# Kernel optimization log

Hardware: AMD Instinct MI355X
Metric: run time of the kernel (lower is better)

The kernel has to match this reference:

```python
import jax, jax.numpy as jnp
import numpy as np

IN_FF = 7  # joints
MASK = np.ones(9, dtype=np.float32)  # [P(3), RPY sin/cos (6)]


def _mlp(x, params):
    # params: list of (W, b); sigmoid after every layer except the last (predict)
    h = x
    for W, b in params[:-1]:
        h = jax.nn.sigmoid(h @ W + b)
    W, b = params[-1]
    return h @ W + b


def _rpy_head(x, params):
    # FeedForwardNet_RPY forward: y -> [sin(y0), cos(y1)], angle = atan2(sin, cos)
    y = _mlp(x, params)
    s = jnp.sin(y[..., 0])
    c = jnp.cos(y[..., 1])
    ang = jnp.arctan2(s, c)
    return jnp.stack([s, c, ang], axis=-1)  # (..., 3)


def setup_inputs():
    key = jax.random.key(0)
    ks = jax.random.split(key, 26)
    m = 16384
    d = {"x": jax.random.normal(ks[0], (m, 2 * IN_FF), jnp.float32)}

    def lin(k, fi, fo, name, i):
        k1, k2 = jax.random.split(k)
        lim = 1.0 / np.sqrt(fi)  # torch Linear default init
        d[name + "_W" + str(i)] = jax.random.uniform(k1, (fi, fo), jnp.float32, -lim, lim)
        d[name + "_b" + str(i)] = jax.random.uniform(k2, (fo,), jnp.float32, -lim, lim)

    idx = 1
    for name, dims in [("pos", [7, 512, 512, 3]), ("roll", [7, 256, 256, 2]),
                       ("pitch", [7, 256, 256, 2]), ("yaw", [7, 256, 256, 2])]:
        for i in range(3):
            lin(ks[idx], dims[i], dims[i + 1], name, i)
            idx += 1
    return d


def _forward(x, pos_p, roll_p, pitch_p, yaw_p):
    mask = jnp.asarray(MASK)
    M_P, M_RPY = mask[:3], mask[3:]
    q, qdot = x[:, :IN_FF], x[:, IN_FF:]

    # position net: forward + per-sample Jacobian (exact, replaces the autograd loop)
    P = _mlp(q, pos_p)                                          # (m, 3)
    J_P = jax.vmap(jax.jacfwd(lambda z: _mlp(z, pos_p)))(q)     # (m, 3, 7)
    vel = jnp.einsum("moi,mi->mo", J_P, qdot)                   # bmm(J_P, jointVels)
    P = P * M_P
    vel = vel * M_P

    heads = []
    for p in (roll_p, pitch_p, yaw_p):
        f = lambda z, p=p: _rpy_head(z, p)
        y = f(q)                                # (m, 3): [sin, cos, angle]
        J = jax.vmap(jax.jacfwd(f))(q)          # (m, 3, 7)
        v = jnp.einsum("moi,mi->mo", J[:, :2, :], qdot)  # (m, 2)
        heads.append((y, J, v))
    (yR, JR, vR), (yPi, JPi, vPi), (yY, JY, vY) = heads

    # order: [roll_sin, pitch_sin, yaw_sin, roll_cos, pitch_cos, yaw_cos]
    RPY = jnp.stack([yR[:, 0], yPi[:, 0], yY[:, 0], yR[:, 1], yPi[:, 1], yY[:, 1]], axis=1) * M_RPY
    vel_RPY = jnp.stack([vR[:, 0], vPi[:, 0], vY[:, 0], vR[:, 1], vPi[:, 1], vY[:, 1]], axis=1) * M_RPY
    J_RPY = jnp.stack([JR[:, 0], JPi[:, 0], JY[:, 0], JR[:, 1], JPi[:, 1], JY[:, 1]], axis=1)  # (m,6,7)

    out = jnp.concatenate([P, RPY, vel, vel_RPY], axis=1)            # (m, 18)
    J_tot = jnp.concatenate([J_P, J_RPY], axis=1)                    # (m, 9, 7)
    out_angles = jnp.concatenate([P, yR[:, 2:3], yPi[:, 2:3], yY[:, 2:3]], axis=1)       # (m, 6)
    J_tot_angles = jnp.concatenate([J_P, JR[:, 2:3], JPi[:, 2:3], JY[:, 2:3]], axis=1)   # (m, 6, 7)
    return out, J_tot, out_angles, J_tot_angles


def reference(x, pos_W0, pos_b0, pos_W1, pos_b1, pos_W2, pos_b2,
              roll_W0, roll_b0, roll_W1, roll_b1, roll_W2, roll_b2,
              pitch_W0, pitch_b0, pitch_W1, pitch_b1, pitch_W2, pitch_b2,
              yaw_W0, yaw_b0, yaw_W1, yaw_b1, yaw_W2, yaw_b2):
    pos_p = [(pos_W0, pos_b0), (pos_W1, pos_b1), (pos_W2, pos_b2)]
    roll_p = [(roll_W0, roll_b0), (roll_W1, roll_b1), (roll_W2, roll_b2)]
    pitch_p = [(pitch_W0, pitch_b0), (pitch_W1, pitch_b1), (pitch_W2, pitch_b2)]
    yaw_p = [(yaw_W0, yaw_b0), (yaw_W1, yaw_b1), (yaw_W2, yaw_b2)]
    return _forward(x, pos_p, roll_p, pitch_p, yaw_p)
```

## Files before the change

kernel.cpp:

```cpp
#include <hip/hip_runtime.h>
#include <math.h>

typedef __attribute__((ext_vector_type(8))) short short8;
typedef __attribute__((ext_vector_type(4))) float floatx4;

__device__ __forceinline__ float sig(float z) { return 1.0f / (1.0f + __expf(-z)); }

__device__ __forceinline__ unsigned short f2bf(float f) {
    unsigned u = __float_as_uint(f);
    u = (u + 0x7FFFu + ((u >> 16) & 1u)) >> 16;
    return (unsigned short)u;
}

__global__ void convert_w1(const float* __restrict__ src, unsigned short* __restrict__ dst,
                           int H, int logH) {
    int idx = blockIdx.x * 256 + threadIdx.x;
    if (idx >= H * H) return;
    int n = idx & (H - 1), k = idx >> logH;
    int KT = H >> 5;
    int blk = (n >> 4) * KT + (k >> 5);
    int lane = ((k >> 3) & 3) * 16 + (n & 15);
    int j = k & 7;
    dst[(blk * 64 + lane) * 8 + j] = f2bf(src[idx]);
}

__global__ __launch_bounds__(256, 2)
void pos_mfma(const float* __restrict__ x,
              const float* __restrict__ W0, const float* __restrict__ b0,
              const float* __restrict__ b1,
              const float* __restrict__ W2, const float* __restrict__ b2,
              const unsigned short* __restrict__ wsW1,
              float* __restrict__ out, int ns)
{
    extern __shared__ unsigned short sA[];
    __shared__ float sB0[512];
    __shared__ float sB1[512];
    __shared__ float sW2[1536];
    __shared__ float sQ[8][8];
    __shared__ float sQd[8][8];
    __shared__ float sAcc[4][64][3];
    __shared__ float sSum[64][3];

    const int tid = threadIdx.x;
    const int m0  = blockIdx.x * 8;

    for (int i = tid; i < 512;  i += 256) { sB0[i] = b0[i]; sB1[i] = b1[i]; }
    for (int i = tid; i < 1536; i += 256) sW2[i] = W2[i];
    if (tid < 112) {
        int m = tid / 14, c = tid % 14;
        float v = x[(m0 + m) * 14 + c];
        if (c < 7) sQ[m][c] = v; else sQd[m][c - 7] = v;
    }
    __syncthreads();

    const float4* W04 = (const float4*)W0;
    #pragma unroll
    for (int t = 0; t < 2; ++t) {
        int item = tid + t * 256;
        int s = item >> 6, k8 = item & 63;
        float q[7], w0v[7][8];
        #pragma unroll
        for (int i = 0; i < 7; i++) {
            q[i] = sQ[s][i];
            float4 a = W04[i * 128 + k8 * 2], b4 = W04[i * 128 + k8 * 2 + 1];
            w0v[i][0]=a.x; w0v[i][1]=a.y; w0v[i][2]=a.z; w0v[i][3]=a.w;
            w0v[i][4]=b4.x; w0v[i][5]=b4.y; w0v[i][6]=b4.z; w0v[i][7]=b4.w;
        }
        float hv[8], dv[8];
        #pragma unroll
        for (int jj = 0; jj < 8; jj++) {
            float z = sB0[k8 * 8 + jj];
            #pragma unroll
            for (int i = 0; i < 7; i++) z = fmaf(q[i], w0v[i][jj], z);
            float h = sig(z);
            hv[jj] = h; dv[jj] = h - h * h;
        }
        int kt = k8 >> 2, kq = k8 & 3, sw = kt & 7;
        int rr0 = s * 8;
        {
            short8 v;
            #pragma unroll
            for (int jj = 0; jj < 8; jj++) v[jj] = (short)f2bf(hv[jj]);
            *(short8*)&sA[((rr0 >> 4) * 16 + kt) * 512 + ((kq * 16 + (rr0 & 15)) ^ sw) * 8] = v;
        }
        #pragma unroll
        for (int i = 0; i < 7; i++) {
            int rr = rr0 + 1 + i;
            short8 v;
            #pragma unroll
            for (int jj = 0; jj < 8; jj++) v[jj] = (short)f2bf(dv[jj] * w0v[i][jj]);
            *(short8*)&sA[((rr >> 4) * 16 + kt) * 512 + ((kq * 16 + (rr & 15)) ^ sw) * 8] = v;
        }
    }
    __syncthreads();

    const int w = tid >> 6, lane = tid & 63;
    const int quad = lane >> 4, col = lane & 15;
    const int srcl = lane & 47;
    const floatx4 z4 = {0.f, 0.f, 0.f, 0.f};

    floatx4 acc[4][8];
    #pragma unroll
    for (int rt = 0; rt < 4; rt++)
        #pragma unroll
        for (int ct = 0; ct < 8; ct++) acc[rt][ct] = z4;

    const short8* bbase = (const short8*)wsW1 + (size_t)(w * 8 * 16) * 64 + lane;

    short8 bufA[8], bufB[8];
    #pragma unroll
    for (int ct = 0; ct < 8; ++ct) bufA[ct] = bbase[(ct * 16) * 64];

    for (int kt2 = 0; kt2 < 16; kt2 += 2) {
        #pragma unroll
        for (int ct = 0; ct < 8; ++ct) bufB[ct] = bbase[(ct * 16 + kt2 + 1) * 64];
        {
            const int kt = kt2, sw = kt & 7;
            short8 afr[4];
            #pragma unroll
            for (int rt = 0; rt < 4; ++rt)
                afr[rt] = *(const short8*)&sA[(rt * 16 + kt) * 512 + (lane ^ sw) * 8];
            #pragma unroll
            for (int ct = 0; ct < 8; ++ct)
                #pragma unroll
                for (int rt = 0; rt < 4; ++rt)
                    acc[rt][ct] = __builtin_amdgcn_mfma_f32_16x16x32_bf16(afr[rt], bufA[ct], acc[rt][ct], 0, 0, 0);
        }
        if (kt2 + 2 < 16) {
            #pragma unroll
            for (int ct = 0; ct < 8; ++ct) bufA[ct] = bbase[(ct * 16 + kt2 + 2) * 64];
        }
        {
            const int kt = kt2 + 1, sw = kt & 7;
            short8 afr[4];
            #pragma unroll
            for (int rt = 0; rt < 4; ++rt)
                afr[rt] = *(const short8*)&sA[(rt * 16 + kt) * 512 + (lane ^ sw) * 8];
            #pragma unroll
            for (int ct = 0; ct < 8; ++ct)
                #pragma unroll
                for (int rt = 0; rt < 4; ++rt)
                    acc[rt][ct] = __builtin_amdgcn_mfma_f32_16x16x32_bf16(afr[rt], bufB[ct], acc[rt][ct], 0, 0, 0);
        }
    }

    float ep[4][4][3];
    #pragma unroll
    for (int a = 0; a < 4; a++) for (int b = 0; b < 4; b++) for (int c = 0; c < 3; c++) ep[a][b][c] = 0.f;

    #pragma unroll
    for (int ct = 0; ct < 8; ++ct) {
        const int n = w * 128 + ct * 16 + col;
        const float b1n = sB1[n];
        const float w20 = sW2[n * 3], w21 = sW2[n * 3 + 1], w22 = sW2[n * 3 + 2];
        #pragma unroll
        for (int rt = 0; rt < 4; ++rt) {
            float z2c = __shfl(acc[rt][ct][0], srcl);
            float h2 = sig(z2c + b1n);
            float d2 = h2 - h2 * h2;
            #pragma unroll
            for (int r = 0; r < 4; ++r) {
                float g = ((quad & 1) == 0 && r == 0) ? h2 : d2 * acc[rt][ct][r];
                ep[rt][r][0] = fmaf(g, w20, ep[rt][r][0]);
                ep[rt][r][1] = fmaf(g, w21, ep[rt][r][1]);
                ep[rt][r][2] = fmaf(g, w22, ep[rt][r][2]);
            }
        }
    }

    #pragma unroll
    for (int mask = 1; mask <= 8; mask <<= 1)
        #pragma unroll
        for (int a = 0; a < 4; a++)
            #pragma unroll
            for (int b = 0; b < 4; b++)
                #pragma unroll
                for (int c = 0; c < 3; c++)
                    ep[a][b][c] += __shfl_xor(ep[a][b][c], mask);
    if (col == 0) {
        #pragma unroll
        for (int rt = 0; rt < 4; ++rt)
            #pragma unroll
            for (int r = 0; r < 4; ++r) {
                int row = rt * 16 + quad * 4 + r;
                sAcc[w][row][0] = ep[rt][r][0];
                sAcc[w][row][1] = ep[rt][r][1];
                sAcc[w][row][2] = ep[rt][r][2];
            }
    }
    __syncthreads();

    const size_t JTOT = (size_t)ns * 18, OUTA = (size_t)ns * 81, JANG = (size_t)ns * 87;
    if (tid < 192) {
        int row = tid / 3, j = tid % 3;
        float v = sAcc[0][row][j] + sAcc[1][row][j] + sAcc[2][row][j] + sAcc[3][row][j];
        int s = row >> 3, i = row & 7;
        size_t M = m0 + s;
        if (i == 0) { v += b2[j]; out[M * 18 + j] = v; out[OUTA + M * 6 + j] = v; }
        else        { out[JTOT + M * 63 + j * 7 + (i - 1)] = v;
                      out[JANG + M * 42 + j * 7 + (i - 1)] = v; }
        sSum[row][j] = v;
    }
    __syncthreads();
    if (tid < 24) {
        int s = tid / 3, j = tid % 3;
        float vel = 0.f;
        #pragma unroll
        for (int i = 0; i < 7; i++) vel = fmaf(sSum[s * 8 + 1 + i][j], sQd[s][i], vel);
        out[(size_t)(m0 + s) * 18 + 9 + j] = vel;
    }
}

__global__ __launch_bounds__(256, 2)
void rpy_mfma(const float* __restrict__ x,
              const float* __restrict__ rW0, const float* __restrict__ rb0,
              const float* __restrict__ rb1,
              const float* __restrict__ rW2, const float* __restrict__ rb2,
              const float* __restrict__ pW0, const float* __restrict__ pb0,
              const float* __restrict__ pb1,
              const float* __restrict__ pW2, const float* __restrict__ pb2,
              const float* __restrict__ yW0, const float* __restrict__ yb0,
              const float* __restrict__ yb1,
              const float* __restrict__ yW2, const float* __restrict__ yb2,
              const unsigned short* __restrict__ wsBase,
              float* __restrict__ out, int ns)
{
    extern __shared__ unsigned short sA[];
    __shared__ float sB0[256];
    __shared__ float sB1[256];
    __shared__ float sW2[512];
    __shared__ float sQ[16][8];
    __shared__ float sQd[16][8];
    __shared__ float sAcc[4][128][2];
    __shared__ float sSum[128][2];

    const int tid = threadIdx.x;
    const int m0  = blockIdx.x * 16;
    const int h   = blockIdx.y;

    const float* W0 = (h == 0) ? rW0 : (h == 1) ? pW0 : yW0;
    const float* b0 = (h == 0) ? rb0 : (h == 1) ? pb0 : yb0;
    const float* b1 = (h == 0) ? rb1 : (h == 1) ? pb1 : yb1;
    const float* W2 = (h == 0) ? rW2 : (h == 1) ? pW2 : yW2;
    const float* b2 = (h == 0) ? rb2 : (h == 1) ? pb2 : yb2;
    const unsigned short* wsW1 = wsBase + 262144 + h * 65536;

    if (tid < 256) { sB0[tid] = b0[tid]; sB1[tid] = b1[tid]; }
    for (int i = tid; i < 512; i += 256) sW2[i] = W2[i];
    if (tid < 224) {
        int m = tid / 14, c = tid % 14;
        float v = x[(m0 + m) * 14 + c];
        if (c < 7) sQ[m][c] = v; else sQd[m][c - 7] = v;
    }
    __syncthreads();

    const float4* W04 = (const float4*)W0;
    #pragma unroll
    for (int t = 0; t < 2; ++t) {
        int item = tid + t * 256;
        int s = item >> 5, k8 = item & 31;
        float q[7], w0v[7][8];
        #pragma unroll
        for (int i = 0; i < 7; i++) {
            q[i] = sQ[s][i];
            float4 a = W04[i * 64 + k8 * 2], b4 = W04[i * 64 + k8 * 2 + 1];
            w0v[i][0]=a.x; w0v[i][1]=a.y; w0v[i][2]=a.z; w0v[i][3]=a.w;
            w0v[i][4]=b4.x; w0v[i][5]=b4.y; w0v[i][6]=b4.z; w0v[i][7]=b4.w;
        }
        float hv[8], dv[8];
        #pragma unroll
        for (int jj = 0; jj < 8; jj++) {
            float z = sB0[k8 * 8 + jj];
            #pragma unroll
            for (int i = 0; i < 7; i++) z = fmaf(q[i], w0v[i][jj], z);
            float hh = sig(z);
            hv[jj] = hh; dv[jj] = hh - hh * hh;
        }
        int kt = k8 >> 2, kq = k8 & 3, sw = kt & 7;
        int rr0 = s * 8;
        {
            short8 v;
            #pragma unroll
            for (int jj = 0; jj < 8; jj++) v[jj] = (short)f2bf(hv[jj]);
            *(short8*)&sA[((rr0 >> 4) * 8 + kt) * 512 + ((kq * 16 + (rr0 & 15)) ^ sw) * 8] = v;
        }
        #pragma unroll
        for (int i = 0; i < 7; i++) {
            int rr = rr0 + 1 + i;
            short8 v;
            #pragma unroll
            for (int jj = 0; jj < 8; jj++) v[jj] = (short)f2bf(dv[jj] * w0v[i][jj]);
            *(short8*)&sA[((rr >> 4) * 8 + kt) * 512 + ((kq * 16 + (rr & 15)) ^ sw) * 8] = v;
        }
    }
    __syncthreads();

    const int w = tid >> 6, lane = tid & 63;
    const int quad = lane >> 4, col = lane & 15;
    const int srcl = lane & 47;
    const floatx4 z4 = {0.f, 0.f, 0.f, 0.f};

    floatx4 acc[8][4];
    #pragma unroll
    for (int rt = 0; rt < 8; rt++)
        #pragma unroll
        for (int ct = 0; ct < 4; ct++) acc[rt][ct] = z4;

    const short8* bbase = (const short8*)wsW1 + (size_t)(w * 4 * 8) * 64 + lane;

    short8 bufA[4], bufB[4];
    #pragma unroll
    for (int ct = 0; ct < 4; ++ct) bufA[ct] = bbase[(ct * 8) * 64];

    for (int kt2 = 0; kt2 < 8; kt2 += 2) {
        #pragma unroll
        for (int ct = 0; ct < 4; ++ct) bufB[ct] = bbase[(ct * 8 + kt2 + 1) * 64];
        {
            const int kt = kt2, sw = kt & 7;
            short8 afr[8];
            #pragma unroll
            for (int rt = 0; rt < 8; ++rt)
                afr[rt] = *(const short8*)&sA[(rt * 8 + kt) * 512 + (lane ^ sw) * 8];
            #pragma unroll
            for (int ct = 0; ct < 4; ++ct)
                #pragma unroll
                for (int rt = 0; rt < 8; ++rt)
                    acc[rt][ct] = __builtin_amdgcn_mfma_f32_16x16x32_bf16(afr[rt], bufA[ct], acc[rt][ct], 0, 0, 0);
        }
        if (kt2 + 2 < 8) {
            #pragma unroll
            for (int ct = 0; ct < 4; ++ct) bufA[ct] = bbase[(ct * 8 + kt2 + 2) * 64];
        }
        {
            const int kt = kt2 + 1, sw = kt & 7;
            short8 afr[8];
            #pragma unroll
            for (int rt = 0; rt < 8; ++rt)
                afr[rt] = *(const short8*)&sA[(rt * 8 + kt) * 512 + (lane ^ sw) * 8];
            #pragma unroll
            for (int ct = 0; ct < 4; ++ct)
                #pragma unroll
                for (int rt = 0; rt < 8; ++rt)
                    acc[rt][ct] = __builtin_amdgcn_mfma_f32_16x16x32_bf16(afr[rt], bufB[ct], acc[rt][ct], 0, 0, 0);
        }
    }

    float ep[8][4][2];
    #pragma unroll
    for (int a = 0; a < 8; a++) for (int b = 0; b < 4; b++) for (int c = 0; c < 2; c++) ep[a][b][c] = 0.f;

    #pragma unroll
    for (int ct = 0; ct < 4; ++ct) {
        const int n = w * 64 + ct * 16 + col;
        const float b1n = sB1[n];
        const float w20 = sW2[n * 2], w21 = sW2[n * 2 + 1];
        #pragma unroll
        for (int rt = 0; rt < 8; ++rt) {
            float z2c = __shfl(acc[rt][ct][0], srcl);
            float h2 = sig(z2c + b1n);
            float d2 = h2 - h2 * h2;
            #pragma unroll
            for (int r = 0; r < 4; ++r) {
                float g = ((quad & 1) == 0 && r == 0) ? h2 : d2 * acc[rt][ct][r];
                ep[rt][r][0] = fmaf(g, w20, ep[rt][r][0]);
                ep[rt][r][1] = fmaf(g, w21, ep[rt][r][1]);
            }
        }
    }

    #pragma unroll
    for (int mask = 1; mask <= 8; mask <<= 1)
        #pragma unroll
        for (int a = 0; a < 8; a++)
            #pragma unroll
            for (int b = 0; b < 4; b++)
                #pragma unroll
                for (int c = 0; c < 2; c++)
                    ep[a][b][c] += __shfl_xor(ep[a][b][c], mask);
    if (col == 0) {
        #pragma unroll
        for (int rt = 0; rt < 8; ++rt)
            #pragma unroll
            for (int r = 0; r < 4; ++r) {
                int row = rt * 16 + quad * 4 + r;
                sAcc[w][row][0] = ep[rt][r][0];
                sAcc[w][row][1] = ep[rt][r][1];
            }
    }
    __syncthreads();

    if (tid < 256) {
        int row = tid >> 1, j = tid & 1;
        float v = sAcc[0][row][j] + sAcc[1][row][j] + sAcc[2][row][j] + sAcc[3][row][j];
        if ((row & 7) == 0) v += b2[j];
        sSum[row][j] = v;
    }
    __syncthreads();

    const size_t JTOT = (size_t)ns * 18, OUTA = (size_t)ns * 81, JANG = (size_t)ns * 87;
    if (tid < 16) {
        int s = tid;
        size_t M = m0 + s;
        float y0 = sSum[s * 8][0], y1 = sSum[s * 8][1];
        float sv = sinf(y0), cv = cosf(y1);
        out[M * 18 + 3 + h] = sv;
        out[M * 18 + 6 + h] = cv;
        out[OUTA + M * 6 + 3 + h] = atan2f(sv, cv);
        float f0 = cosf(y0), f1 = -sinf(y1);
        float inv = 1.0f / fmaf(sv, sv, cv * cv);
        float v0 = 0.f, v1 = 0.f;
        #pragma unroll
        for (int i = 0; i < 7; i++) {
            float r0 = f0 * sSum[s * 8 + 1 + i][0];
            float r1 = f1 * sSum[s * 8 + 1 + i][1];
            out[JTOT + M * 63 + (3 + h) * 7 + i] = r0;
            out[JTOT + M * 63 + (6 + h) * 7 + i] = r1;
            out[JANG + M * 42 + (3 + h) * 7 + i] = (cv * r0 - sv * r1) * inv;
            v0 = fmaf(r0, sQd[s][i], v0);
            v1 = fmaf(r1, sQd[s][i], v1);
        }
        out[M * 18 + 12 + h] = v0;
        out[M * 18 + 15 + h] = v1;
    }
}

extern "C" void kernel_launch(void* const* d_in, const int* in_sizes, int n_in,
                              void* d_out, int out_size, void* d_ws, size_t ws_size,
                              hipStream_t stream) {
    (void)n_in; (void)out_size; (void)ws_size;
    const float* x = (const float*)d_in[0];
    float* out = (float*)d_out;
    unsigned short* ws = (unsigned short*)d_ws;
    const int ns = in_sizes[0] / 14;

    convert_w1<<<dim3((512 * 512) / 256), 256, 0, stream>>>((const float*)d_in[3],  ws,          512, 9);
    convert_w1<<<dim3((256 * 256) / 256), 256, 0, stream>>>((const float*)d_in[9],  ws + 262144, 256, 8);
    convert_w1<<<dim3((256 * 256) / 256), 256, 0, stream>>>((const float*)d_in[15], ws + 327680, 256, 8);
    convert_w1<<<dim3((256 * 256) / 256), 256, 0, stream>>>((const float*)d_in[21], ws + 393216, 256, 8);

    pos_mfma<<<dim3(ns / 8), 256, 65536, stream>>>(
        x,
        (const float*)d_in[1], (const float*)d_in[2],
        (const float*)d_in[4],
        (const float*)d_in[5], (const float*)d_in[6],
        ws, out, ns);

    rpy_mfma<<<dim3(ns / 16, 3), 256, 65536, stream>>>(
        x,
        (const float*)d_in[7],  (const float*)d_in[8],  (const float*)d_in[10],
        (const float*)d_in[11], (const float*)d_in[12],
        (const float*)d_in[13], (const float*)d_in[14], (const float*)d_in[16],
        (const float*)d_in[17], (const float*)d_in[18],
        (const float*)d_in[19], (const float*)d_in[20], (const float*)d_in[22],
        (const float*)d_in[23], (const float*)d_in[24],
        ws, out, ns);
}
```

Baseline: 338.4 us.

## Fuse position and RPY MLP kernels into one interleaved launch

Merges the separate position-net and RPY-head kernels into one kernel whose 1D grid assigns, in each group of five blocks, two blocks to position tiles and three to the roll/pitch/yaw heads. Shared-memory scratch for the two paths is overlaid with a union. The aim is to remove one kernel launch and the serialization between the two passes, so both kinds of work run on the GPU at the same time and fill its tail better. In exchange the fused kernel's register allocation is set by the heavier branch, which could lower occupancy or add divergence overhead.

```diff
diff --git a/kernel.cpp b/kernel.cpp
--- a/kernel.cpp
+++ b/kernel.cpp
@@ -24,403 +24,388 @@
     dst[(blk * 64 + lane) * 8 + j] = f2bf(src[idx]);
 }
 
+struct PosS {
+    float B0[512], B1[512], W2[1536];
+    float Q[8][8], Qd[8][8];
+    float Acc[4][64][3], Sum[64][3];
+};
+struct RpyS {
+    float B0[256], B1[256], W2[512];
+    float Q[16][8], Qd[16][8];
+    float Acc[4][128][2], Sum[128][2];
+};
+
 __global__ __launch_bounds__(256, 2)
-void pos_mfma(const float* __restrict__ x,
-              const float* __restrict__ W0, const float* __restrict__ b0,
-              const float* __restrict__ b1,
-              const float* __restrict__ W2, const float* __restrict__ b2,
-              const unsigned short* __restrict__ wsW1,
-              float* __restrict__ out, int ns)
+void fused_mfma(const float* __restrict__ x,
+                const float* __restrict__ pW0, const float* __restrict__ pb0,
+                const float* __restrict__ pb1,
+                const float* __restrict__ pW2, const float* __restrict__ pb2,
+                const float* __restrict__ rW0_, const float* __restrict__ rb0_,
+                const float* __restrict__ rb1_,
+                const float* __restrict__ rW2_, const float* __restrict__ rb2_,
+                const float* __restrict__ piW0, const float* __restrict__ pib0,
+                const float* __restrict__ pib1,
+                const float* __restrict__ piW2, const float* __restrict__ pib2,
+                const float* __restrict__ yW0, const float* __restrict__ yb0,
+                const float* __restrict__ yb1,
+                const float* __restrict__ yW2, const float* __restrict__ yb2,
+                const unsigned short* __restrict__ wsBase,
+                float* __restrict__ out, int ns)
 {
     extern __shared__ unsigned short sA[];
-    __shared__ float sB0[512];
-    __shared__ float sB1[512];
-    __shared__ float sW2[1536];
-    __shared__ float sQ[8][8];
-    __shared__ float sQd[8][8];
-    __shared__ float sAcc[4][64][3];
-    __shared__ float sSum[64][3];
+    __shared__ union { PosS p; RpyS r; } sU;
 
     const int tid = threadIdx.x;
-    const int m0  = blockIdx.x * 8;
-
-    for (int i = tid; i < 512;  i += 256) { sB0[i] = b0[i]; sB1[i] = b1[i]; }
-    for (int i = tid; i < 1536; i += 256) sW2[i] = W2[i];
-    if (tid < 112) {
-        int m = tid / 14, c = tid % 14;
-        float v = x[(m0 + m) * 14 + c];
-        if (c < 7) sQ[m][c] = v; else sQd[m][c - 7] = v;
-    }
-    __syncthreads();
-
-    const float4* W04 = (const float4*)W0;
-    #pragma unroll
-    for (int t = 0; t < 2; ++t) {
-        int item = tid + t * 256;
-        int s = item >> 6, k8 = item & 63;
-        float q[7], w0v[7][8];
-        #pragma unroll
-        for (int i = 0; i < 7; i++) {
-            q[i] = sQ[s][i];
-            float4 a = W04[i * 128 + k8 * 2], b4 = W04[i * 128 + k8 * 2 + 1];
-            w0v[i][0]=a.x; w0v[i][1]=a.y; w0v[i][2]=a.z; w0v[i][3]=a.w;
-            w0v[i][4]=b4.x; w0v[i][5]=b4.y; w0v[i][6]=b4.z; w0v[i][7]=b4.w;
-        }
-        float hv[8], dv[8];
-        #pragma unroll
-        for (int jj = 0; jj < 8; jj++) {
-            float z = sB0[k8 * 8 + jj];
-            #pragma unroll
-            for (int i = 0; i < 7; i++) z = fmaf(q[i], w0v[i][jj], z);
-            float h = sig(z);
-            hv[jj] = h; dv[jj] = h - h * h;
-        }
-        int kt = k8 >> 2, kq = k8 & 3, sw = kt & 7;
-        int rr0 = s * 8;
-        {
-            short8 v;
-            #pragma unroll
-            for (int jj = 0; jj < 8; jj++) v[jj] = (short)f2bf(hv[jj]);
-            *(short8*)&sA[((rr0 >> 4) * 16 + kt) * 512 + ((kq * 16 + (rr0 & 15)) ^ sw) * 8] = v;
-        }
-        #pragma unroll
-        for (int i = 0; i < 7; i++) {
-            int rr = rr0 + 1 + i;
-            short8 v;
-            #pragma unroll
-            for (int jj = 0; jj < 8; jj++) v[jj] = (short)f2bf(dv[jj] * w0v[i][jj]);
-            *(short8*)&sA[((rr >> 4) * 16 + kt) * 512 + ((kq * 16 + (rr & 15)) ^ sw) * 8] = v;
-        }
-    }
-    __syncthreads();
-
+    const int f = blockIdx.x;
+    const int g = f / 5, r5 = f % 5;
+    const size_t JTOT = (size_t)ns * 18, OUTA = (size_t)ns * 81, JANG = (size_t)ns * 87;
+    const floatx4 z4 = {0.f, 0.f, 0.f, 0.f};
     const int w = tid >> 6, lane = tid & 63;
     const int quad = lane >> 4, col = lane & 15;
     const int srcl = lane & 47;
-    const floatx4 z4 = {0.f, 0.f, 0.f, 0.f};
-
-    floatx4 acc[4][8];
-    #pragma unroll
-    for (int rt = 0; rt < 4; rt++)
-        #pragma unroll
-        for (int ct = 0; ct < 8; ct++) acc[rt][ct] = z4;
-
-    const short8* bbase = (const short8*)wsW1 + (size_t)(w * 8 * 16) * 64 + lane;
-
-    short8 bufA[8], bufB[8];
-    #pragma unroll
-    for (int ct = 0; ct < 8; ++ct) bufA[ct] = bbase[(ct * 16) * 64];
-
-    for (int kt2 = 0; kt2 < 16; kt2 += 2) {
-        #pragma unroll
-        for (int ct = 0; ct < 8; ++ct) bufB[ct] = bbase[(ct * 16 + kt2 + 1) * 64];
-        {
-            const int kt = kt2, sw = kt & 7;
-            short8 afr[4];
+
+    if (r5 < 2) {
+        const int m0 = (g * 2 + r5) * 8;
+        const unsigned short* wsW1 = wsBase;
+
+        for (int i = tid; i < 512;  i += 256) { sU.p.B0[i] = pb0[i]; sU.p.B1[i] = pb1[i]; }
+        for (int i = tid; i < 1536; i += 256) sU.p.W2[i] = pW2[i];
+        if (tid < 112) {
+            int m = tid / 14, c = tid % 14;
+            float v = x[(m0 + m) * 14 + c];
+            if (c < 7) sU.p.Q[m][c] = v; else sU.p.Qd[m][c - 7] = v;
+        }
+        __syncthreads();
+
+        const float4* W04 = (const float4*)pW0;
+        #pragma unroll
+        for (int t = 0; t < 2; ++t) {
+            int item = tid + t * 256;
+            int s = item >> 6, k8 = item & 63;
+            float q[7], w0v[7][8];
+            #pragma unroll
+            for (int i = 0; i < 7; i++) {
+                q[i] = sU.p.Q[s][i];
+                float4 a = W04[i * 128 + k8 * 2], b4 = W04[i * 128 + k8 * 2 + 1];
+                w0v[i][0]=a.x; w0v[i][1]=a.y; w0v[i][2]=a.z; w0v[i][3]=a.w;
+                w0v[i][4]=b4.x; w0v[i][5]=b4.y; w0v[i][6]=b4.z; w0v[i][7]=b4.w;
+            }
+            float hv[8], dv[8];
+            #pragma unroll
+            for (int jj = 0; jj < 8; jj++) {
+                float z = sU.p.B0[k8 * 8 + jj];
+                #pragma unroll
+                for (int i = 0; i < 7; i++) z = fmaf(q[i], w0v[i][jj], z);
+                float h = sig(z);
+                hv[jj] = h; dv[jj] = h - h * h;
+            }
+            int kt = k8 >> 2, kq = k8 & 3, sw = kt & 7;
+            int rr0 = s * 8;
+            {
+                short8 v;
+                #pragma unroll
+                for (int jj = 0; jj < 8; jj++) v[jj] = (short)f2bf(hv[jj]);
+                *(short8*)&sA[((rr0 >> 4) * 16 + kt) * 512 + ((kq * 16 + (rr0 & 15)) ^ sw) * 8] = v;
+            }
+            #pragma unroll
+            for (int i = 0; i < 7; i++) {
+                int rr = rr0 + 1 + i;
+                short8 v;
+                #pragma unroll
+                for (int jj = 0; jj < 8; jj++) v[jj] = (short)f2bf(dv[jj] * w0v[i][jj]);
+                *(short8*)&sA[((rr >> 4) * 16 + kt) * 512 + ((kq * 16 + (rr & 15)) ^ sw) * 8] = v;
+            }
+        }
+        __syncthreads();
+
+        floatx4 acc[4][8];
+        #pragma unroll
+        for (int rt = 0; rt < 4; rt++)
+            #pragma unroll
+            for (int ct = 0; ct < 8; ct++) acc[rt][ct] = z4;
+
+        const short8* bbase = (const short8*)wsW1 + (size_t)(w * 8 * 16) * 64 + lane;
+        short8 bufA[8], bufB[8];
+        #pragma unroll
+        for (int ct = 0; ct < 8; ++ct) bufA[ct] = bbase[(ct * 16) * 64];
+
+        for (int kt2 = 0; kt2 < 16; kt2 += 2) {
+            #pragma unroll
+            for (int ct = 0; ct < 8; ++ct) bufB[ct] = bbase[(ct * 16 + kt2 + 1) * 64];
+            {
+                const int kt = kt2, sw = kt & 7;
+                short8 afr[4];
+                #pragma unroll
+                for (int rt = 0; rt < 4; ++rt)
+                    afr[rt] = *(const short8*)&sA[(rt * 16 + kt) * 512 + (lane ^ sw) * 8];
+                #pragma unroll
+                for (int ct = 0; ct < 8; ++ct)
+                    #pragma unroll
+                    for (int rt = 0; rt < 4; ++rt)
+                        acc[rt][ct] = __builtin_amdgcn_mfma_f32_16x16x32_bf16(afr[rt], bufA[ct], acc[rt][ct], 0, 0, 0);
+            }
+            if (kt2 + 2 < 16) {
+                #pragma unroll
+                for (int ct = 0; ct < 8; ++ct) bufA[ct] = bbase[(ct * 16 + kt2 + 2) * 64];
+            }
+            {
+                const int kt = kt2 + 1, sw = kt & 7;
+                short8 afr[4];
+                #pragma unroll
+                for (int rt = 0; rt < 4; ++rt)
+                    afr[rt] = *(const short8*)&sA[(rt * 16 + kt) * 512 + (lane ^ sw) * 8];
+                #pragma unroll
+                for (int ct = 0; ct < 8; ++ct)
+                    #pragma unroll
+                    for (int rt = 0; rt < 4; ++rt)
+                        acc[rt][ct] = __builtin_amdgcn_mfma_f32_16x16x32_bf16(afr[rt], bufB[ct], acc[rt][ct], 0, 0, 0);
+            }
+        }
+
+        float ep[4][4][3];
+        #pragma unroll
+        for (int a = 0; a < 4; a++) for (int b = 0; b < 4; b++) for (int c = 0; c < 3; c++) ep[a][b][c] = 0.f;
+
+        #pragma unroll
+        for (int ct = 0; ct < 8; ++ct) {
+            const int n = w * 128 + ct * 16 + col;
+            const float b1n = sU.p.B1[n];
+            const float w20 = sU.p.W2[n * 3], w21 = sU.p.W2[n * 3 + 1], w22 = sU.p.W2[n * 3 + 2];
+            #pragma unroll
+            for (int rt = 0; rt < 4; ++rt) {
+                float z2c = __shfl(acc[rt][ct][0], srcl);
+                float h2 = sig(z2c + b1n);
+                float d2 = h2 - h2 * h2;
+                #pragma unroll
+                for (int r = 0; r < 4; ++r) {
+                    float gg = ((quad & 1) == 0 && r == 0) ? h2 : d2 * acc[rt][ct][r];
+                    ep[rt][r][0] = fmaf(gg, w20, ep[rt][r][0]);
+                    ep[rt][r][1] = fmaf(gg, w21, ep[rt][r][1]);
+                    ep[rt][r][2] = fmaf(gg, w22, ep[rt][r][2]);
+                }
+            }
+        }
+
+        #pragma unroll
+        for (int mask = 1; mask <= 8; mask <<= 1)
+            #pragma unroll
+            for (int a = 0; a < 4; a++)
+                #pragma unroll
+                for (int b = 0; b < 4; b++)
+                    #pragma unroll
+                    for (int c = 0; c < 3; c++)
+                        ep[a][b][c] += __shfl_xor(ep[a][b][c], mask);
+        if (col == 0) {
             #pragma unroll
             for (int rt = 0; rt < 4; ++rt)
-                afr[rt] = *(const short8*)&sA[(rt * 16 + kt) * 512 + (lane ^ sw) * 8];
-            #pragma unroll
-            for (int ct = 0; ct < 8; ++ct)
-                #pragma unroll
-                for (int rt = 0; rt < 4; ++rt)
-                    acc[rt][ct] = __builtin_amdgcn_mfma_f32_16x16x32_bf16(afr[rt], bufA[ct], acc[rt][ct], 0, 0, 0);
-        }
-        if (kt2 + 2 < 16) {
-            #pragma unroll
-            for (int ct = 0; ct < 8; ++ct) bufA[ct] = bbase[(ct * 16 + kt2 + 2) * 64];
-        }
-        {
-            const int kt = kt2 + 1, sw = kt & 7;
-            short8 afr[4];
-            #pragma unroll
-            for (int rt = 0; rt < 4; ++rt)
-                afr[rt] = *(const short8*)&sA[(rt * 16 + kt) * 512 + (lane ^ sw) * 8];
-            #pragma unroll
-            for (int ct = 0; ct < 8; ++ct)
-                #pragma unroll
-                for (int rt = 0; rt < 4; ++rt)
-                    acc[rt][ct] = __builtin_amdgcn_mfma_f32_16x16x32_bf16(afr[rt], bufB[ct], acc[rt][ct], 0, 0, 0);
-        }
-    }
-
-    float ep[4][4][3];
-    #pragma unroll
-    for (int a = 0; a < 4; a++) for (int b = 0; b < 4; b++) for (int c = 0; c < 3; c++) ep[a][b][c] = 0.f;
-
-    #pragma unroll
-    for (int ct = 0; ct < 8; ++ct) {
-        const int n = w * 128 + ct * 16 + col;
-        const float b1n = sB1[n];
-        const float w20 = sW2[n * 3], w21 = sW2[n * 3 + 1], w22 = sW2[n * 3 + 2];
-        #pragma unroll
-        for (int rt = 0; rt < 4; ++rt) {
-            float z2c = __shfl(acc[rt][ct][0], srcl);
-            float h2 = sig(z2c + b1n);
-            float d2 = h2 - h2 * h2;
-            #pragma unroll
-            for (int r = 0; r < 4; ++r) {
-                float g = ((quad & 1) == 0 && r == 0) ? h2 : d2 * acc[rt][ct][r];
-                ep[rt][r][0] = fmaf(g, w20, ep[rt][r][0]);
-                ep[rt][r][1] = fmaf(g, w21, ep[rt][r][1]);
-                ep[rt][r][2] = fmaf(g, w22, ep[rt][r][2]);
-            }
-        }
-    }
-
-    #pragma unroll
-    for (int mask = 1; mask <= 8; mask <<= 1)
-        #pragma unroll
-        for (int a = 0; a < 4; a++)
-            #pragma unroll
-            for (int b = 0; b < 4; b++)
-                #pragma unroll
-                for (int c = 0; c < 3; c++)
-                    ep[a][b][c] += __shfl_xor(ep[a][b][c], mask);
-    if (col == 0) {
-        #pragma unroll
-        for (int rt = 0; rt < 4; ++rt)
-            #pragma unroll
-            for (int r = 0; r < 4; ++r) {
-                int row = rt * 16 + quad * 4 + r;
-                sAcc[w][row][0] = ep[rt][r][0];
-                sAcc[w][row][1] = ep[rt][r][1];
-                sAcc[w][row][2] = ep[rt][r][2];
-            }
-    }
-    __syncthreads();
-
-    const size_t JTOT = (size_t)ns * 18, OUTA = (size_t)ns * 81, JANG = (size_t)ns * 87;
-    if (tid < 192) {
-        int row = tid / 3, j = tid % 3;
-        float v = sAcc[0][row][j] + sAcc[1][row][j] + sAcc[2][row][j] + sAcc[3][row][j];
-        int s = row >> 3, i = row & 7;
-        size_t M = m0 + s;
-        if (i == 0) { v += b2[j]; out[M * 18 + j] = v; out[OUTA + M * 6 + j] = v; }
-        else        { out[JTOT + M * 63 + j * 7 + (i - 1)] = v;
-                      out[JANG + M * 42 + j * 7 + (i - 1)] = v; }
-        sSum[row][j] = v;
-    }
-    __syncthreads();
-    if (tid < 24) {
-        int s = tid / 3, j = tid % 3;
-        float vel = 0.f;
-        #pragma unroll
-        for (int i = 0; i < 7; i++) vel = fmaf(sSum[s * 8 + 1 + i][j], sQd[s][i], vel);
-        out[(size_t)(m0 + s) * 18 + 9 + j] = vel;
-    }
-}
-
-__global__ __launch_bounds__(256, 2)
-void rpy_mfma(const float* __restrict__ x,
-              const float* __restrict__ rW0, const float* __restrict__ rb0,
-              const float* __restrict__ rb1,
-              const float* __restrict__ rW2, const float* __restrict__ rb2,
-              const float* __restrict__ pW0, const float* __restrict__ pb0,
-              const float* __restrict__ pb1,
-              const float* __restrict__ pW2, const float* __restrict__ pb2,
-              const float* __restrict__ yW0, const float* __restrict__ yb0,
-              const float* __restrict__ yb1,
-              const float* __restrict__ yW2, const float* __restrict__ yb2,
-              const unsigned short* __restrict__ wsBase,
-              float* __restrict__ out, int ns)
-{
-    extern __shared__ unsigned short sA[];
-    __shared__ float sB0[256];
-    __shared__ float sB1[256];
-    __shared__ float sW2[512];
-    __shared__ float sQ[16][8];
-    __shared__ float sQd[16][8];
-    __shared__ float sAcc[4][128][2];
-    __shared__ float sSum[128][2];
-
-    const int tid = threadIdx.x;
-    const int m0  = blockIdx.x * 16;
-    const int h   = blockIdx.y;
-
-    const float* W0 = (h == 0) ? rW0 : (h == 1) ? pW0 : yW0;
-    const float* b0 = (h == 0) ? rb0 : (h == 1) ? pb0 : yb0;
-    const float* b1 = (h == 0) ? rb1 : (h == 1) ? pb1 : yb1;
-    const float* W2 = (h == 0) ? rW2 : (h == 1) ? pW2 : yW2;
-    const float* b2 = (h == 0) ? rb2 : (h == 1) ? pb2 : yb2;
-    const unsigned short* wsW1 = wsBase + 262144 + h * 65536;
-
-    if (tid < 256) { sB0[tid] = b0[tid]; sB1[tid] = b1[tid]; }
-    for (int i = tid; i < 512; i += 256) sW2[i] = W2[i];
-    if (tid < 224) {
-        int m = tid / 14, c = tid % 14;
-        float v = x[(m0 + m) * 14 + c];
-        if (c < 7) sQ[m][c] = v; else sQd[m][c - 7] = v;
-    }
-    __syncthreads();
-
-    const float4* W04 = (const float4*)W0;
-    #pragma unroll
-    for (int t = 0; t < 2; ++t) {
-        int item = tid + t * 256;
-        int s = item >> 5, k8 = item & 31;
-        float q[7], w0v[7][8];
-        #pragma unroll
-        for (int i = 0; i < 7; i++) {
-            q[i] = sQ[s][i];
-            float4 a = W04[i * 64 + k8 * 2], b4 = W04[i * 64 + k8 * 2 + 1];
-            w0v[i][0]=a.x; w0v[i][1]=a.y; w0v[i][2]=a.z; w0v[i][3]=a.w;
-            w0v[i][4]=b4.x; w0v[i][5]=b4.y; w0v[i][6]=b4.z; w0v[i][7]=b4.w;
-        }
-        float hv[8], dv[8];
-        #pragma unroll
-        for (int jj = 0; jj < 8; jj++) {
-            float z = sB0[k8 * 8 + jj];
-            #pragma unroll
-            for (int i = 0; i < 7; i++) z = fmaf(q[i], w0v[i][jj], z);
-            float hh = sig(z);
-            hv[jj] = hh; dv[jj] = hh - hh * hh;
-        }
-        int kt = k8 >> 2, kq = k8 & 3, sw = kt & 7;
-        int rr0 = s * 8;
-        {
-            short8 v;
-            #pragma unroll
-            for (int jj = 0; jj < 8; jj++) v[jj] = (short)f2bf(hv[jj]);
-            *(short8*)&sA[((rr0 >> 4) * 8 + kt) * 512 + ((kq * 16 + (rr0 & 15)) ^ sw) * 8] = v;
-        }
-        #pragma unroll
-        for (int i = 0; i < 7; i++) {
-            int rr = rr0 + 1 + i;
-            short8 v;
-            #pragma unroll
-            for (int jj = 0; jj < 8; jj++) v[jj] = (short)f2bf(dv[jj] * w0v[i][jj]);
-            *(short8*)&sA[((rr >> 4) * 8 + kt) * 512 + ((kq * 16 + (rr & 15)) ^ sw) * 8] = v;
-        }
-    }
-    __syncthreads();
-
-    const int w = tid >> 6, lane = tid & 63;
-    const int quad = lane >> 4, col = lane & 15;
-    const int srcl = lane & 47;
-    const floatx4 z4 = {0.f, 0.f, 0.f, 0.f};
-
-    floatx4 acc[8][4];
-    #pragma unroll
-    for (int rt = 0; rt < 8; rt++)
-        #pragma unroll
-        for (int ct = 0; ct < 4; ct++) acc[rt][ct] = z4;
-
-    const short8* bbase = (const short8*)wsW1 + (size_t)(w * 4 * 8) * 64 + lane;
-
-    short8 bufA[4], bufB[4];
-    #pragma unroll
-    for (int ct = 0; ct < 4; ++ct) bufA[ct] = bbase[(ct * 8) * 64];
-
-    for (int kt2 = 0; kt2 < 8; kt2 += 2) {
-        #pragma unroll
-        for (int ct = 0; ct < 4; ++ct) bufB[ct] = bbase[(ct * 8 + kt2 + 1) * 64];
-        {
-            const int kt = kt2, sw = kt & 7;
-            short8 afr[8];
+                #pragma unroll
+                for (int r = 0; r < 4; ++r) {
+                    int row = rt * 16 + quad * 4 + r;
+                    sU.p.Acc[w][row][0] = ep[rt][r][0];
+                    sU.p.Acc[w][row][1] = ep[rt][r][1];
+                    sU.p.Acc[w][row][2] = ep[rt][r][2];
+                }
+        }
+        __syncthreads();
+
+        if (tid < 192) {
+            int row = tid / 3, j = tid % 3;
+            float v = sU.p.Acc[0][row][j] + sU.p.Acc[1][row][j] + sU.p.Acc[2][row][j] + sU.p.Acc[3][row][j];
+            int s = row >> 3, i = row & 7;
+            size_t M = m0 + s;
+            if (i == 0) { v += pb2[j]; out[M * 18 + j] = v; out[OUTA + M * 6 + j] = v; }
+            else        { out[JTOT + M * 63 + j * 7 + (i - 1)] = v;
+                          out[JANG + M * 42 + j * 7 + (i - 1)] = v; }
+            sU.p.Sum[row][j] = v;
+        }
+        __syncthreads();
+        if (tid < 24) {
+            int s = tid / 3, j = tid % 3;
+            float vel = 0.f;
+            #pragma unroll
+            for (int i = 0; i < 7; i++) vel = fmaf(sU.p.Sum[s * 8 + 1 + i][j], sU.p.Qd[s][i], vel);
+            out[(size_t)(m0 + s) * 18 + 9 + j] = vel;
+        }
+    } else {
+        const int h = r5 - 2;
+        const int m0 = g * 16;
+        const float* W0 = (h == 0) ? rW0_ : (h == 1) ? piW0 : yW0;
+        const float* b0 = (h == 0) ? rb0_ : (h == 1) ? pib0 : yb0;
+        const float* b1 = (h == 0) ? rb1_ : (h == 1) ? pib1 : yb1;
+        const float* W2 = (h == 0) ? rW2_ : (h == 1) ? piW2 : yW2;
+        const float* b2 = (h == 0) ? rb2_ : (h == 1) ? pib2 : yb2;
+        const unsigned short* wsW1 = wsBase + 262144 + h * 65536;
+
+        if (tid < 256) { sU.r.B0[tid] = b0[tid]; sU.r.B1[tid] = b1[tid]; }
+        for (int i = tid; i < 512; i += 256) sU.r.W2[i] = W2[i];
+        if (tid < 224) {
+            int m = tid / 14, c = tid % 14;
+            float v = x[(m0 + m) * 14 + c];
+            if (c < 7) sU.r.Q[m][c] = v; else sU.r.Qd[m][c - 7] = v;
+        }
+        __syncthreads();
+
+        const float4* W04 = (const float4*)W0;
+        #pragma unroll
+        for (int t = 0; t < 2; ++t) {
+            int item = tid + t * 256;
+            int s = item >> 5, k8 = item & 31;
+            float q[7], w0v[7][8];
+            #pragma unroll
+            for (int i = 0; i < 7; i++) {
+                q[i] = sU.r.Q[s][i];
+                float4 a = W04[i * 64 + k8 * 2], b4 = W04[i * 64 + k8 * 2 + 1];
+                w0v[i][0]=a.x; w0v[i][1]=a.y; w0v[i][2]=a.z; w0v[i][3]=a.w;
+                w0v[i][4]=b4.x; w0v[i][5]=b4.y; w0v[i][6]=b4.z; w0v[i][7]=b4.w;
+            }
+            float hv[8], dv[8];
+            #pragma unroll
+            for (int jj = 0; jj < 8; jj++) {
+                float z = sU.r.B0[k8 * 8 + jj];
+                #pragma unroll
+                for (int i = 0; i < 7; i++) z = fmaf(q[i], w0v[i][jj], z);
+                float hh = sig(z);
+                hv[jj] = hh; dv[jj] = hh - hh * hh;
+            }
+            int kt = k8 >> 2, kq = k8 & 3, sw = kt & 7;
+            int rr0 = s * 8;
+            {
+                short8 v;
+                #pragma unroll
+                for (int jj = 0; jj < 8; jj++) v[jj] = (short)f2bf(hv[jj]);
+                *(short8*)&sA[((rr0 >> 4) * 8 + kt) * 512 + ((kq * 16 + (rr0 & 15)) ^ sw) * 8] = v;
+            }
+            #pragma unroll
+            for (int i = 0; i < 7; i++) {
+                int rr = rr0 + 1 + i;
+                short8 v;
+                #pragma unroll
+                for (int jj = 0; jj < 8; jj++) v[jj] = (short)f2bf(dv[jj] * w0v[i][jj]);
+                *(short8*)&sA[((rr >> 4) * 8 + kt) * 512 + ((kq * 16 + (rr & 15)) ^ sw) * 8] = v;
+            }
+        }
+        __syncthreads();
+
+        floatx4 acc[8][4];
+        #pragma unroll
+        for (int rt = 0; rt < 8; rt++)
+            #pragma unroll
+            for (int ct = 0; ct < 4; ct++) acc[rt][ct] = z4;
+
+        const short8* bbase = (const short8*)wsW1 + (size_t)(w * 4 * 8) * 64 + lane;
+        short8 bufA[4], bufB[4];
+        #pragma unroll
+        for (int ct = 0; ct < 4; ++ct) bufA[ct] = bbase[(ct * 8) * 64];
+
+        for (int kt2 = 0; kt2 < 8; kt2 += 2) {
+            #pragma unroll
+            for (int ct = 0; ct < 4; ++ct) bufB[ct] = bbase[(ct * 8 + kt2 + 1) * 64];
+            {
+                const int kt = kt2, sw = kt & 7;
+                short8 afr[8];
+                #pragma unroll
+                for (int rt = 0; rt < 8; ++rt)
+                    afr[rt] = *(const short8*)&sA[(rt * 8 + kt) * 512 + (lane ^ sw) * 8];
+                #pragma unroll
+                for (int ct = 0; ct < 4; ++ct)
+                    #pragma unroll
+                    for (int rt = 0; rt < 8; ++rt)
+                        acc[rt][ct] = __builtin_amdgcn_mfma_f32_16x16x32_bf16(afr[rt], bufA[ct], acc[rt][ct], 0, 0, 0);
+            }
+            if (kt2 + 2 < 8) {
+                #pragma unroll
+                for (int ct = 0; ct < 4; ++ct) bufA[ct] = bbase[(ct * 8 + kt2 + 2) * 64];
+            }
+            {
+                const int kt = kt2 + 1, sw = kt & 7;
+                short8 afr[8];
+                #pragma unroll
+                for (int rt = 0; rt < 8; ++rt)
+                    afr[rt] = *(const short8*)&sA[(rt * 8 + kt) * 512 + (lane ^ sw) * 8];
+                #pragma unroll
+                for (int ct = 0; ct < 4; ++ct)
+                    #pragma unroll
+                    for (int rt = 0; rt < 8; ++rt)
+                        acc[rt][ct] = __builtin_amdgcn_mfma_f32_16x16x32_bf16(afr[rt], bufB[ct], acc[rt][ct], 0, 0, 0);
+            }
+        }
+
+        float ep[8][4][2];
+        #pragma unroll
+        for (int a = 0; a < 8; a++) for (int b = 0; b < 4; b++) for (int c = 0; c < 2; c++) ep[a][b][c] = 0.f;
+
+        #pragma unroll
+        for (int ct = 0; ct < 4; ++ct) {
+            const int n = w * 64 + ct * 16 + col;
+            const float b1n = sU.r.B1[n];
+            const float w20 = sU.r.W2[n * 2], w21 = sU.r.W2[n * 2 + 1];
+            #pragma unroll
+            for (int rt = 0; rt < 8; ++rt) {
+                float z2c = __shfl(acc[rt][ct][0], srcl);
+                float h2 = sig(z2c + b1n);
+                float d2 = h2 - h2 * h2;
+                #pragma unroll
+                for (int r = 0; r < 4; ++r) {
+                    float gg = ((quad & 1) == 0 && r == 0) ? h2 : d2 * acc[rt][ct][r];
+                    ep[rt][r][0] = fmaf(gg, w20, ep[rt][r][0]);
+                    ep[rt][r][1] = fmaf(gg, w21, ep[rt][r][1]);
+                }
+            }
+        }
+
+        #pragma unroll
+        for (int mask = 1; mask <= 8; mask <<= 1)
+            #pragma unroll
+            for (int a = 0; a < 8; a++)
+                #pragma unroll
+                for (int b = 0; b < 4; b++)
+                    #pragma unroll
+                    for (int c = 0; c < 2; c++)
+                        ep[a][b][c] += __shfl_xor(ep[a][b][c], mask);
+        if (col == 0) {
             #pragma unroll
             for (int rt = 0; rt < 8; ++rt)
-                afr[rt] = *(const short8*)&sA[(rt * 8 + kt) * 512 + (lane ^ sw) * 8];
-            #pragma unroll
-            for (int ct = 0; ct < 4; ++ct)
-                #pragma unroll
-                for (int rt = 0; rt < 8; ++rt)
-                    acc[rt][ct] = __builtin_amdgcn_mfma_f32_16x16x32_bf16(afr[rt], bufA[ct], acc[rt][ct], 0, 0, 0);
-        }
-        if (kt2 + 2 < 8) {
-            #pragma unroll
-            for (int ct = 0; ct < 4; ++ct) bufA[ct] = bbase[(ct * 8 + kt2 + 2) * 64];
-        }
-        {
-            const int kt = kt2 + 1, sw = kt & 7;
-            short8 afr[8];
-            #pragma unroll
-            for (int rt = 0; rt < 8; ++rt)
-                afr[rt] = *(const short8*)&sA[(rt * 8 + kt) * 512 + (lane ^ sw) * 8];
-            #pragma unroll
-            for (int ct = 0; ct < 4; ++ct)
-                #pragma unroll
-                for (int rt = 0; rt < 8; ++rt)
-                    acc[rt][ct] = __builtin_amdgcn_mfma_f32_16x16x32_bf16(afr[rt], bufB[ct], acc[rt][ct], 0, 0, 0);
-        }
-    }
-
-    float ep[8][4][2];
-    #pragma unroll
-    for (int a = 0; a < 8; a++) for (int b = 0; b < 4; b++) for (int c = 0; c < 2; c++) ep[a][b][c] = 0.f;
-
-    #pragma unroll
-    for (int ct = 0; ct < 4; ++ct) {
-        const int n = w * 64 + ct * 16 + col;
-        const float b1n = sB1[n];
-        const float w20 = sW2[n * 2], w21 = sW2[n * 2 + 1];
-        #pragma unroll
-        for (int rt = 0; rt < 8; ++rt) {
-            float z2c = __shfl(acc[rt][ct][0], srcl);
-            float h2 = sig(z2c + b1n);
-            float d2 = h2 - h2 * h2;
-            #pragma unroll
-            for (int r = 0; r < 4; ++r) {
-                float g = ((quad & 1) == 0 && r == 0) ? h2 : d2 * acc[rt][ct][r];
-                ep[rt][r][0] = fmaf(g, w20, ep[rt][r][0]);
-                ep[rt][r][1] = fmaf(g, w21, ep[rt][r][1]);
-            }
-        }
-    }
-
-    #pragma unroll
-    for (int mask = 1; mask <= 8; mask <<= 1)
-        #pragma unroll
-        for (int a = 0; a < 8; a++)
-            #pragma unroll
-            for (int b = 0; b < 4; b++)
-                #pragma unroll
-                for (int c = 0; c < 2; c++)
-                    ep[a][b][c] += __shfl_xor(ep[a][b][c], mask);
-    if (col == 0) {
-        #pragma unroll
-        for (int rt = 0; rt < 8; ++rt)
-            #pragma unroll
-            for (int r = 0; r < 4; ++r) {
-                int row = rt * 16 + quad * 4 + r;
-                sAcc[w][row][0] = ep[rt][r][0];
-                sAcc[w][row][1] = ep[rt][r][1];
-            }
-    }
-    __syncthreads();
-
-    if (tid < 256) {
-        int row = tid >> 1, j = tid & 1;
-        float v = sAcc[0][row][j] + sAcc[1][row][j] + sAcc[2][row][j] + sAcc[3][row][j];
-        if ((row & 7) == 0) v += b2[j];
-        sSum[row][j] = v;
-    }
-    __syncthreads();
-
-    const size_t JTOT = (size_t)ns * 18, OUTA = (size_t)ns * 81, JANG = (size_t)ns * 87;
-    if (tid < 16) {
-        int s = tid;
-        size_t M = m0 + s;
-        float y0 = sSum[s * 8][0], y1 = sSum[s * 8][1];
-        float sv = sinf(y0), cv = cosf(y1);
-        out[M * 18 + 3 + h] = sv;
-        out[M * 18 + 6 + h] = cv;
-        out[OUTA + M * 6 + 3 + h] = atan2f(sv, cv);
-        float f0 = cosf(y0), f1 = -sinf(y1);
-        float inv = 1.0f / fmaf(sv, sv, cv * cv);
-        float v0 = 0.f, v1 = 0.f;
-        #pragma unroll
-        for (int i = 0; i < 7; i++) {
-            float r0 = f0 * sSum[s * 8 + 1 + i][0];
-            float r1 = f1 * sSum[s * 8 + 1 + i][1];
-            out[JTOT + M * 63 + (3 + h) * 7 + i] = r0;
-            out[JTOT + M * 63 + (6 + h) * 7 + i] = r1;
-            out[JANG + M * 42 + (3 + h) * 7 + i] = (cv * r0 - sv * r1) * inv;
-            v0 = fmaf(r0, sQd[s][i], v0);
-            v1 = fmaf(r1, sQd[s][i], v1);
-        }
-        out[M * 18 + 12 + h] = v0;
-        out[M * 18 + 15 + h] = v1;
+                #pragma unroll
+                for (int r = 0; r < 4; ++r) {
+                    int row = rt * 16 + quad * 4 + r;
+                    sU.r.Acc[w][row][0] = ep[rt][r][0];
+                    sU.r.Acc[w][row][1] = ep[rt][r][1];
+                }
+        }
+        __syncthreads();
+
+        if (tid < 256) {
+            int row = tid >> 1, j = tid & 1;
+            float v = sU.r.Acc[0][row][j] + sU.r.Acc[1][row][j] + sU.r.Acc[2][row][j] + sU.r.Acc[3][row][j];
+            if ((row & 7) == 0) v += b2[j];
+            sU.r.Sum[row][j] = v;
+        }
+        __syncthreads();
+
+        if (tid < 16) {
+            int s = tid;
+            size_t M = m0 + s;
+            float y0 = sU.r.Sum[s * 8][0], y1 = sU.r.Sum[s * 8][1];
+            float sv = sinf(y0), cv = cosf(y1);
+            out[M * 18 + 3 + h] = sv;
+            out[M * 18 + 6 + h] = cv;
+            out[OUTA + M * 6 + 3 + h] = atan2f(sv, cv);
+            float f0 = cosf(y0), f1 = -sinf(y1);
+            float inv = 1.0f / fmaf(sv, sv, cv * cv);
+            float v0 = 0.f, v1 = 0.f;
+            #pragma unroll
+            for (int i = 0; i < 7; i++) {
+                float r0 = f0 * sU.r.Sum[s * 8 + 1 + i][0];
+                float r1 = f1 * sU.r.Sum[s * 8 + 1 + i][1];
+                out[JTOT + M * 63 + (3 + h) * 7 + i] = r0;
+                out[JTOT + M * 63 + (6 + h) * 7 + i] = r1;
+                out[JANG + M * 42 + (3 + h) * 7 + i] = (cv * r0 - sv * r1) * inv;
+                v0 = fmaf(r0, sU.r.Qd[s][i], v0);
+                v1 = fmaf(r1, sU.r.Qd[s][i], v1);
+            }
+            out[M * 18 + 12 + h] = v0;
+            out[M * 18 + 15 + h] = v1;
+        }
     }
 }
 
@@ -438,15 +423,10 @@
     convert_w1<<<dim3((256 * 256) / 256), 256, 0, stream>>>((const float*)d_in[15], ws + 327680, 256, 8);
     convert_w1<<<dim3((256 * 256) / 256), 256, 0, stream>>>((const float*)d_in[21], ws + 393216, 256, 8);
 
-    pos_mfma<<<dim3(ns / 8), 256, 65536, stream>>>(
+    fused_mfma<<<dim3((ns / 8 / 2) * 5), 256, 65536, stream>>>(
         x,
-        (const float*)d_in[1], (const float*)d_in[2],
-        (const float*)d_in[4],
-        (const float*)d_in[5], (const float*)d_in[6],
-        ws, out, ns);
-
-    rpy_mfma<<<dim3(ns / 16, 3), 256, 65536, stream>>>(
-        x,
+        (const float*)d_in[1],  (const float*)d_in[2],  (const float*)d_in[4],
+        (const float*)d_in[5],  (const float*)d_in[6],
         (const float*)d_in[7],  (const float*)d_in[8],  (const float*)d_in[10],
         (const float*)d_in[11], (const float*)d_in[12],
         (const float*)d_in[13], (const float*)d_in[14], (const float*)d_in[16],
```

Result: no change. 335.9 us (-0.7%).
